# Kernel tuning notes

Measured on AMD Instinct MI355X. Metric: run time of the kernel, lower is better.

The kernel has to match this reference:

```python
import jax, jax.numpy as jnp
import numpy as np

BITS = 4
GROUP = 128
IN_F = 4096
OUT_F = 4096
MAXQ = (1 << BITS) - 1  # 15
TOKENS = 8192


def setup_inputs() -> dict:
    key = jax.random.key(0)
    k1, k2, k3, k4, k5 = jax.random.split(key, 5)
    x = jax.random.normal(k1, (TOKENS, IN_F), dtype=jnp.float32)
    # packed 4-bit weights: 8 values per int32 word along the input dim
    qweight = jax.random.randint(k2, (IN_F // 32 * BITS, OUT_F), 0, 2147483647, dtype=jnp.int32)
    # packed 4-bit zero points: 8 values per int32 word along the output dim
    qzeros = jax.random.randint(k3, (IN_F // GROUP, OUT_F // 32 * BITS), 0, 2147483647, dtype=jnp.int32)
    scales = jax.random.uniform(k4, (IN_F // GROUP, OUT_F), dtype=jnp.float32, minval=0.001, maxval=0.02)
    bias = jax.random.normal(k5, (OUT_F,), dtype=jnp.float32)
    g_idx = (jnp.arange(IN_F) // GROUP).astype(jnp.int32)
    return {"x": x, "qweight": qweight, "qzeros": qzeros, "scales": scales, "bias": bias, "g_idx": g_idx}


def _dequantize(qweight, qzeros, scales, g_idx):
    # shift amounts for the 32//BITS = 8 nibbles packed per int32 word
    shifts = jnp.arange(0, 32, BITS, dtype=jnp.int32)
    # unpack weights: [IN//32*BITS, 8, OUT] -> [IN, OUT], values in [0, MAXQ]
    w = (qweight[:, None, :] >> shifts[None, :, None]) & MAXQ
    w = w.reshape(IN_F, OUT_F)
    # unpack zero points: [G, OUT//32*BITS, 8] -> [G, OUT]
    z = (qzeros[:, :, None] >> shifts[None, None, :]) & MAXQ
    z = z.reshape(scales.shape[0], OUT_F)
    # per-group dequant: W = s[g] * (w - z[g])  (tritonv2 dequant, no +1 on zeros)
    gi = g_idx.astype(jnp.int32)
    W = scales[gi] * (w.astype(scales.dtype) - z[gi].astype(scales.dtype))
    return W  # [IN, OUT]


def reference(x, qweight, qzeros, scales, bias, g_idx):
    W = _dequantize(qweight, qzeros, scales, g_idx)
    out = x @ W + bias  # [TOKENS, OUT]
    return out
```

## Files before the change

### kernel.cpp

```cpp
#include <hip/hip_runtime.h>
#include <hip/hip_bf16.h>
#include <stdint.h>

#define TOKENS 8192
#define IN_F   4096
#define OUT_F  4096
#define GROUP  128

typedef __attribute__((ext_vector_type(4))) int   i32x4;
typedef __attribute__((ext_vector_type(4))) float f32x4;

__global__ __launch_bounds__(256) void k_prep(
    const float* __restrict__ x, int8_t* __restrict__ xq,
    float* __restrict__ xs, const int* __restrict__ qweight,
    const int* __restrict__ qzeros, const float* __restrict__ scales,
    int8_t* __restrict__ wq, float* __restrict__ sw) {
  __shared__ float smax[16][17];
  __shared__ float red[4];
  const int bid = blockIdx.x;
  const int t = threadIdx.x;

  if (bid < 256) {
    const int n0 = bid * 16;
    const int col = t & 15;
    const int seg = t >> 4;
    const int n = n0 + col;

    int zloc[2];
    float sloc[2];
    float m = 0.f;
#pragma unroll
    for (int i = 0; i < 2; ++i) {
      const int g = seg * 2 + i;
      const unsigned zw =
          ((const unsigned*)qzeros)[(size_t)g * (OUT_F / 8) + (n >> 3)];
      const int z = (int)((zw >> ((n & 7) * 4)) & 15u);
      const float s = scales[(size_t)g * OUT_F + n];
      zloc[i] = z;
      sloc[i] = s;
      m = fmaxf(m, s * (float)(z > 15 - z ? z : 15 - z));
    }
    smax[col][seg] = m;
    __syncthreads();
    float Sw = 0.f;
#pragma unroll
    for (int ss = 0; ss < 16; ++ss) Sw = fmaxf(Sw, smax[col][ss]);
    Sw /= 127.f;
    if (seg == 0) sw[n] = Sw;
    const float inv = 1.f / Sw;

#pragma unroll
    for (int i = 0; i < 2; ++i) {
      const int g = seg * 2 + i;
      const int z = zloc[i];
      const float f = sloc[i] * inv;
#pragma unroll
      for (int kw = 0; kw < 16; ++kw) {
        const unsigned w =
            ((const unsigned*)qweight)[(size_t)(g * 16 + kw) * OUT_F + n];
        unsigned lo = 0, hi = 0;
#pragma unroll
        for (int j = 0; j < 8; ++j) {
          const int q = (int)((w >> (4 * j)) & 15u);
          const int v = __float2int_rn(f * (float)(q - z));
          const unsigned b = (unsigned)(v & 255);
          if (j < 4)
            lo |= b << (8 * j);
          else
            hi |= b << (8 * (j - 4));
        }
        uint2 pk = {lo, hi};
        *(uint2*)(wq + (size_t)n * IN_F + (size_t)(g * 16 + kw) * 8) = pk;
      }
    }
  } else {
    const int row = bid - 256;
    const float4* xr = (const float4*)(x + (size_t)row * IN_F) + t * 4;
    float f[16];
    *(float4*)&f[0] = xr[0];
    *(float4*)&f[4] = xr[1];
    *(float4*)&f[8] = xr[2];
    *(float4*)&f[12] = xr[3];
    float am = 0.f;
#pragma unroll
    for (int j = 0; j < 16; ++j) am = fmaxf(am, fabsf(f[j]));
#pragma unroll
    for (int off = 32; off; off >>= 1) am = fmaxf(am, __shfl_xor(am, off));
    if ((t & 63) == 0) red[t >> 6] = am;
    __syncthreads();
    am = fmaxf(fmaxf(red[0], red[1]), fmaxf(red[2], red[3]));
    am = fmaxf(am, 1e-8f);
    const float inv = 127.f / am;
    if (t == 0) xs[row] = am / 127.f;
    union {
      i32x4 v;
      int8_t c[16];
    } u;
#pragma unroll
    for (int j = 0; j < 16; ++j) u.c[j] = (int8_t)__float2int_rn(f[j] * inv);
    ((i32x4*)(xq + (size_t)row * IN_F))[t] = u.v;
  }
}

__device__ inline void gload_lds16(const void* g, void* l) {
  __builtin_amdgcn_global_load_lds(
      (const __attribute__((address_space(1))) void*)g,
      (__attribute__((address_space(3))) void*)l, 16, 0, 0);
}

#define STAGE_T(buf, tile)                                                    \
  do {                                                                        \
    _Pragma("unroll") for (int i_ = 0; i_ < 4; ++i_) {                        \
      gload_lds16(Ag + goffS[i_] + (size_t)((tile) & 31) * 128,               \
                  smem + (buf)*32768 + ldsS[i_]);                             \
    }                                                                         \
    _Pragma("unroll") for (int i_ = 0; i_ < 4; ++i_) {                        \
      gload_lds16(Bg + goffS[i_] + (size_t)((tile) & 31) * 128,               \
                  smem + (buf)*32768 + 16384 + ldsS[i_]);                     \
    }                                                                         \
  } while (0)

#define PHASE(bufc, T)                                                        \
  do {                                                                        \
    _Pragma("unroll") for (int nf_ = 0; nf_ < 4; ++nf_) {                     \
      const char* p_ =                                                        \
          smem + (bufc)*32768 + 16384 + (wc * 64 + nf_ * 16 + fr) * 128;      \
      bF[nf_][0] = *(const i32x4*)(p_ + csw0);                                \
      bF[nf_][1] = *(const i32x4*)(p_ + csw1);                                \
    }                                                                         \
    _Pragma("unroll") for (int mf_ = 0; mf_ < 4; ++mf_) {                     \
      const char* p_ = smem + (bufc)*32768 + (wr * 64 + mf_ * 16 + fr) * 128; \
      aF[mf_][0] = *(const i32x4*)(p_ + csw0);                                \
      aF[mf_][1] = *(const i32x4*)(p_ + csw1);                                \
    }                                                                         \
    asm volatile("s_waitcnt lgkmcnt(0)" ::: "memory");                        \
    __builtin_amdgcn_sched_barrier(0);                                        \
    __builtin_amdgcn_s_barrier();          \
    STAGE_T(bufc, (T) + 2);                   \
    __builtin_amdgcn_s_setprio(1);                                            \
    _Pragma("unroll") for (int nf_ = 0; nf_ < 4; ++nf_)                       \
        _Pragma("unroll") for (int mf_ = 0; mf_ < 4; ++mf_) {                 \
      iacc[mf_][nf_] = __builtin_amdgcn_mfma_i32_16x16x64_i8(                 \
          aF[mf_][0], bF[nf_][0], iacc[mf_][nf_], 0, 0, 0);                   \
    }                                                                         \
    _Pragma("unroll") for (int nf_ = 0; nf_ < 4; ++nf_)                       \
        _Pragma("unroll") for (int mf_ = 0; mf_ < 4; ++mf_) {                 \
      iacc[mf_][nf_] = __builtin_amdgcn_mfma_i32_16x16x64_i8(                 \
          aF[mf_][1], bF[nf_][1], iacc[mf_][nf_], 0, 0, 0);                   \
    }                                                                         \
    __builtin_amdgcn_s_setprio(0);                                            \
    __builtin_amdgcn_sched_barrier(0);                                        \
    asm volatile("s_waitcnt vmcnt(8)" ::: "memory");                          \
    __builtin_amdgcn_s_barrier();                                             \
  } while (0)

__global__ __launch_bounds__(256, 2) void k_gemm_i8(
    const int8_t* __restrict__ xq,
    const int8_t* __restrict__ wq,
    const float* __restrict__ sw,
    const float* __restrict__ xs,
    const float* __restrict__ bias,
    float* __restrict__ out) {
  extern __shared__ __align__(16) char smem[];

  const int bidx = blockIdx.x;
  const int xcd = bidx & 7;
  const int slot = bidx >> 3;
  const int bm = slot >> 2;
  const int bn = xcd * 4 + (slot & 3);
  const int m0 = bm * 128;
  const int n0 = bn * 128;

  const int t = threadIdx.x;
  const int lane = t & 63;
  const int wid = t >> 6;
  const int wr = wid >> 1;
  const int wc = wid & 1;
  const int fr = lane & 15;
  const int hq = lane >> 4;

  const int csw0 = (hq ^ (fr & 7)) * 16;
  const int csw1 = ((hq ^ 4) ^ (fr & 7)) * 16;

  int goffS[4], ldsS[4];
#pragma unroll
  for (int i = 0; i < 4; ++i) {
    const int srow = wid * 32 + i * 8 + (lane >> 3);
    const int sch = (lane & 7) ^ (srow & 7);
    goffS[i] = srow * IN_F + sch * 16;
    ldsS[i] = (wid * 4 + i) * 1024;
  }

  const char* Ag = (const char*)(xq + (size_t)m0 * IN_F);
  const char* Bg = (const char*)(wq + (size_t)n0 * IN_F);

  i32x4 iacc[4][4];
#pragma unroll
  for (int i = 0; i < 4; ++i)
#pragma unroll
    for (int j = 0; j < 4; ++j) iacc[i][j] = (i32x4){0, 0, 0, 0};

  i32x4 aF[4][2];
  i32x4 bF[4][2];

  STAGE_T(0, 0);
  STAGE_T(1, 1);
  asm volatile("s_waitcnt vmcnt(8) lgkmcnt(0)" ::: "memory");
  __builtin_amdgcn_s_barrier();

#pragma unroll 1
  for (int it = 0; it < 16; ++it) {
    const int T = 2 * it;
    PHASE(0, T);
    PHASE(1, T + 1);
  }

  float swv[4], bv[4];
#pragma unroll
  for (int nf = 0; nf < 4; ++nf) {
    const int n = n0 + wc * 64 + nf * 16 + fr;
    swv[nf] = sw[n];
    bv[nf] = bias[n];
  }
#pragma unroll
  for (int mf = 0; mf < 4; ++mf) {
#pragma unroll
    for (int r = 0; r < 4; ++r) {
      const int m = m0 + wr * 64 + mf * 16 + hq * 4 + r;
      const float xsv = xs[m];
      float* o = out + (size_t)m * OUT_F + n0;
#pragma unroll
      for (int nf = 0; nf < 4; ++nf) {
        o[wc * 64 + nf * 16 + fr] =
            xsv * swv[nf] * (float)iacc[mf][nf][r] + bv[nf];
      }
    }
  }
}

extern "C" void kernel_launch(void* const* d_in, const int* in_sizes, int n_in,
                              void* d_out, int out_size, void* d_ws,
                              size_t ws_size, hipStream_t stream) {
  const float* x = (const float*)d_in[0];
  const int* qweight = (const int*)d_in[1];
  const int* qzeros = (const int*)d_in[2];
  const float* scales = (const float*)d_in[3];
  const float* bias = (const float*)d_in[4];
  float* out = (float*)d_out;

  int8_t* xq = (int8_t*)d_ws;
  int8_t* wq = xq + (size_t)TOKENS * IN_F;
  float* xs = (float*)(wq + (size_t)OUT_F * IN_F);
  float* sw = xs + TOKENS;

  (void)hipFuncSetAttribute(reinterpret_cast<const void*>(&k_gemm_i8),
                            hipFuncAttributeMaxDynamicSharedMemorySize, 65536);

  k_prep<<<256 + TOKENS, 256, 0, stream>>>(x, xq, xs, qweight, qzeros, scales,
                                           wq, sw);
  k_gemm_i8<<<(TOKENS / 128) * (OUT_F / 128), 256, 65536, stream>>>(
      xq, wq, sw, xs, bias, out);
}
```

Before: 181.5 us.

## Halve GEMM K-tile to 64 to cut LDS and raise occupancy to 3 blocks

Shrinks the int8 GEMM K-tile from 128 to 64 bytes per stage, which halves LDS use per block to 32 KB and halves the A/B fragment registers. The LDS swizzle and staging addresses are reworked for 64-byte rows, and launch bounds move to 3 blocks per CU. The goal is more resident waves to hide memory latency, at the cost of twice as many barriers and pipeline phases per output tile and a shallower prefetch distance in bytes.

```diff
diff --git a/kernel.cpp b/kernel.cpp
--- a/kernel.cpp
+++ b/kernel.cpp
@@ -110,28 +110,25 @@
 
 #define STAGE_T(buf, tile)                                                    \
   do {                                                                        \
-    _Pragma("unroll") for (int i_ = 0; i_ < 4; ++i_) {                        \
-      gload_lds16(Ag + goffS[i_] + (size_t)((tile) & 31) * 128,               \
-                  smem + (buf)*32768 + ldsS[i_]);                             \
-    }                                                                         \
-    _Pragma("unroll") for (int i_ = 0; i_ < 4; ++i_) {                        \
-      gload_lds16(Bg + goffS[i_] + (size_t)((tile) & 31) * 128,               \
-                  smem + (buf)*32768 + 16384 + ldsS[i_]);                     \
+    _Pragma("unroll") for (int r_ = 0; r_ < 2; ++r_) {                        \
+      gload_lds16(Ag + goffS[r_] + (size_t)((tile) & 63) * 64,                \
+                  smem + (buf)*16384 + ldsS[r_]);                             \
+    }                                                                         \
+    _Pragma("unroll") for (int r_ = 0; r_ < 2; ++r_) {                        \
+      gload_lds16(Bg + goffS[r_] + (size_t)((tile) & 63) * 64,                \
+                  smem + (buf)*16384 + 8192 + ldsS[r_]);                      \
     }                                                                         \
   } while (0)
 
 #define PHASE(bufc, T)                                                        \
   do {                                                                        \
+    const char* aB_ = smem + (bufc)*16384 + (wr * 64 + fr) * 64;              \
+    const char* bB_ = smem + (bufc)*16384 + 8192 + (wc * 64 + fr) * 64;       \
+    _Pragma("unroll") for (int mf_ = 0; mf_ < 4; ++mf_) {                     \
+      aF[mf_] = *(const i32x4*)(aB_ + mf_ * 1024 + csw);                      \
+    }                                                                         \
     _Pragma("unroll") for (int nf_ = 0; nf_ < 4; ++nf_) {                     \
-      const char* p_ =                                                        \
-          smem + (bufc)*32768 + 16384 + (wc * 64 + nf_ * 16 + fr) * 128;      \
-      bF[nf_][0] = *(const i32x4*)(p_ + csw0);                                \
-      bF[nf_][1] = *(const i32x4*)(p_ + csw1);                                \
-    }                                                                         \
-    _Pragma("unroll") for (int mf_ = 0; mf_ < 4; ++mf_) {                     \
-      const char* p_ = smem + (bufc)*32768 + (wr * 64 + mf_ * 16 + fr) * 128; \
-      aF[mf_][0] = *(const i32x4*)(p_ + csw0);                                \
-      aF[mf_][1] = *(const i32x4*)(p_ + csw1);                                \
+      bF[nf_] = *(const i32x4*)(bB_ + nf_ * 1024 + csw);                      \
     }                                                                         \
     asm volatile("s_waitcnt lgkmcnt(0)" ::: "memory");                        \
     __builtin_amdgcn_sched_barrier(0);                                        \
@@ -141,20 +138,15 @@
     _Pragma("unroll") for (int nf_ = 0; nf_ < 4; ++nf_)                       \
         _Pragma("unroll") for (int mf_ = 0; mf_ < 4; ++mf_) {                 \
       iacc[mf_][nf_] = __builtin_amdgcn_mfma_i32_16x16x64_i8(                 \
-          aF[mf_][0], bF[nf_][0], iacc[mf_][nf_], 0, 0, 0);                   \
-    }                                                                         \
-    _Pragma("unroll") for (int nf_ = 0; nf_ < 4; ++nf_)                       \
-        _Pragma("unroll") for (int mf_ = 0; mf_ < 4; ++mf_) {                 \
-      iacc[mf_][nf_] = __builtin_amdgcn_mfma_i32_16x16x64_i8(                 \
-          aF[mf_][1], bF[nf_][1], iacc[mf_][nf_], 0, 0, 0);                   \
+          aF[mf_], bF[nf_], iacc[mf_][nf_], 0, 0, 0);                         \
     }                                                                         \
     __builtin_amdgcn_s_setprio(0);                                            \
     __builtin_amdgcn_sched_barrier(0);                                        \
-    asm volatile("s_waitcnt vmcnt(8)" ::: "memory");                          \
+    asm volatile("s_waitcnt vmcnt(4)" ::: "memory");                          \
     __builtin_amdgcn_s_barrier();                                             \
   } while (0)
 
-__global__ __launch_bounds__(256, 2) void k_gemm_i8(
+__global__ __launch_bounds__(256, 3) void k_gemm_i8(
     const int8_t* __restrict__ xq,
     const int8_t* __restrict__ wq,
     const float* __restrict__ sw,
@@ -179,16 +171,16 @@
   const int fr = lane & 15;
   const int hq = lane >> 4;
 
-  const int csw0 = (hq ^ (fr & 7)) * 16;
-  const int csw1 = ((hq ^ 4) ^ (fr & 7)) * 16;
-
-  int goffS[4], ldsS[4];
-#pragma unroll
-  for (int i = 0; i < 4; ++i) {
-    const int srow = wid * 32 + i * 8 + (lane >> 3);
-    const int sch = (lane & 7) ^ (srow & 7);
-    goffS[i] = srow * IN_F + sch * 16;
-    ldsS[i] = (wid * 4 + i) * 1024;
+  const int csw = (hq ^ ((fr >> 1) & 3)) * 16;
+
+  int goffS[2], ldsS[2];
+#pragma unroll
+  for (int r = 0; r < 2; ++r) {
+    const int c = r * 256 + t;
+    const int srow = c >> 2;
+    const int sch = (c & 3) ^ ((srow >> 1) & 3);
+    goffS[r] = srow * IN_F + sch * 16;
+    ldsS[r] = (r * 256 + wid * 64) * 16;
   }
 
   const char* Ag = (const char*)(xq + (size_t)m0 * IN_F);
@@ -200,16 +192,16 @@
 #pragma unroll
     for (int j = 0; j < 4; ++j) iacc[i][j] = (i32x4){0, 0, 0, 0};
 
-  i32x4 aF[4][2];
-  i32x4 bF[4][2];
+  i32x4 aF[4];
+  i32x4 bF[4];
 
   STAGE_T(0, 0);
   STAGE_T(1, 1);
-  asm volatile("s_waitcnt vmcnt(8) lgkmcnt(0)" ::: "memory");
+  asm volatile("s_waitcnt vmcnt(4) lgkmcnt(0)" ::: "memory");
   __builtin_amdgcn_s_barrier();
 
 #pragma unroll 1
-  for (int it = 0; it < 16; ++it) {
+  for (int it = 0; it < 32; ++it) {
     const int T = 2 * it;
     PHASE(0, T);
     PHASE(1, T + 1);
@@ -254,10 +246,10 @@
   float* sw = xs + TOKENS;
 
   (void)hipFuncSetAttribute(reinterpret_cast<const void*>(&k_gemm_i8),
-                            hipFuncAttributeMaxDynamicSharedMemorySize, 65536);
+                            hipFuncAttributeMaxDynamicSharedMemorySize, 32768);
 
   k_prep<<<256 + TOKENS, 256, 0, stream>>>(x, xq, xs, qweight, qzeros, scales,
                                            wq, sw);
-  k_gemm_i8<<<(TOKENS / 128) * (OUT_F / 128), 256, 65536, stream>>>(
+  k_gemm_i8<<<(TOKENS / 128) * (OUT_F / 128), 256, 32768, stream>>>(
       xq, wq, sw, xs, bias, out);
 }
```

Result: slower. 221.9 us (+22.3%).
